# Kernel optimization log

Hardware: AMD Instinct MI355X
Metric: run time of the kernel (lower is better)

Reference implementation:

```python
import jax, jax.numpy as jnp
import numpy as np

N = 50000   # nodes
E = 800000  # edges (before self loops)
F = 128     # in_dim
H = 4       # heads
C = 32      # hidden_dim per head
HC = H * C  # 128 == F
L = 3       # n_layers
G = 64      # graphs in batch
OUT = 64    # out_dim
NEG_SLOPE = 0.2


def setup_inputs() -> dict:
    key = jax.random.key(0)
    ks = jax.random.split(key, 12)
    s = 0.1
    x = jax.random.normal(ks[0], (N, F), jnp.float32)
    src = jax.random.randint(ks[1], (E,), 0, N, dtype=jnp.int32)
    dst = jax.random.randint(ks[2], (E,), 0, N, dtype=jnp.int32)
    # even split into G graphs so no graph is empty (segment_max safe)
    batch = (jnp.arange(N, dtype=jnp.int32) * G // N).astype(jnp.int32)
    Ws = jax.random.normal(ks[3], (L, HC, HC), jnp.float32) * s       # layer0 in=F=HC
    att_src = jax.random.normal(ks[4], (L, H, C), jnp.float32) * s
    att_dst = jax.random.normal(ks[5], (L, H, C), jnp.float32) * s
    conv_b = jnp.zeros((L, HC), jnp.float32)
    gate_W = jax.random.normal(ks[6], (L + 1, HC, 1), jnp.float32) * s
    gate_b = jnp.zeros((L + 1,), jnp.float32)
    lin_W = jax.random.normal(ks[7], (L + 1, HC, OUT), jnp.float32) * s
    lin_b = jnp.zeros((L + 1, OUT), jnp.float32)
    h_weights = jnp.ones((L + 1,), jnp.float32) / (L + 1)
    h0 = jax.random.normal(ks[8], (1,), jnp.float32)
    beta = jax.random.normal(ks[9], (OUT,), jnp.float32) * s
    pool_w = jnp.ones((3,), jnp.float32) / 3.0
    return dict(x=x, src=src, dst=dst, batch=batch, Ws=Ws, att_src=att_src,
                att_dst=att_dst, conv_b=conv_b, gate_W=gate_W, gate_b=gate_b,
                lin_W=lin_W, lin_b=lin_b, h_weights=h_weights, h0=h0,
                beta=beta, pool_w=pool_w)


def _seg_softmax(e, idx, n):
    # numerically stable softmax within segments
    m = jax.ops.segment_max(e, idx, num_segments=n)
    m = jnp.where(jnp.isfinite(m), m, 0.0)
    ex = jnp.exp(e - m[idx])
    s = jax.ops.segment_sum(ex, idx, num_segments=n)
    return ex / (s[idx] + 1e-16)


def _gat_layer(x, src, dst, W, a_src, a_dst, b):
    h = (x @ W).reshape(N, H, C)               # [N,H,C]
    al_s = jnp.sum(h * a_src, axis=-1)         # [N,H]
    al_d = jnp.sum(h * a_dst, axis=-1)         # [N,H]
    e = jax.nn.leaky_relu(al_s[src] + al_d[dst], NEG_SLOPE)  # [E+N,H]
    alpha = _seg_softmax(e, dst, N)            # softmax over incoming edges
    msg = h[src] * alpha[..., None]            # [E+N,H,C]
    out = jax.ops.segment_sum(msg, dst, num_segments=N)
    return out.reshape(N, HC) + b


def _pool_block(x, gw, gb, pool_w, batch, counts):
    gate = jax.nn.sigmoid(x @ gw + gb)[:, 0]          # [N]
    a = _seg_softmax(gate, batch, G)                  # per-graph attention
    p_att = jax.ops.segment_sum(a[:, None] * x, batch, num_segments=G)
    p_mean = jax.ops.segment_sum(x, batch, num_segments=G) / counts[:, None]
    p_max = jax.ops.segment_max(x, batch, num_segments=G)
    return pool_w[0] * p_att + pool_w[1] * p_mean + pool_w[2] * p_max


def reference(x, src, dst, batch, Ws, att_src, att_dst, conv_b, gate_W,
              gate_b, lin_W, lin_b, h_weights, h0, beta, pool_w):
    loops = jnp.arange(N, dtype=src.dtype)
    src_sl = jnp.concatenate([src, loops])
    dst_sl = jnp.concatenate([dst, loops])
    counts = jax.ops.segment_sum(jnp.ones((N,), x.dtype), batch, num_segments=G)
    out = jnp.zeros((G, OUT), x.dtype)
    for i in range(L):
        p = _pool_block(x, gate_W[i], gate_b[i], pool_w, batch, counts)
        out = out + h_weights[i] * (p @ lin_W[i] + lin_b[i])
        x = _gat_layer(x, src_sl, dst_sl, Ws[i], att_src[i], att_dst[i], conv_b[i])
        if i != L - 1:
            x = jax.nn.relu(x)
    p = _pool_block(x, gate_W[L], gate_b[L], pool_w, batch, counts)
    out = out + h_weights[L] * (p @ lin_W[L] + lin_b[L])
    risk_score = out @ beta + h0[0]   # [G]
    return risk_score
```

## Files before the change

### kernel.cpp

```cpp
#include <hip/hip_runtime.h>
#include <hip/hip_fp16.h>
#include <math.h>

#define N_NODES 50000
#define N_EDGES 800000
#define HC 128
#define NH 4
#define NG 64
#define NOUT 64
#define NLAYERS 3
#define POOL_CHUNKS 16
#define CAST_BLOCKS (N_NODES * HC / 4 / 256)
#define PREPW_BLOCKS (NLAYERS * HC * HC / 256)
#define NBKT ((N_NODES + 127) / 128)
#define PB_BLOCKS ((N_EDGES + 4095) / 4096)
#define GEMM_BLOCKS ((N_NODES + 15) / 16)
#define POOL2_BLOCKS (NG * POOL_CHUNKS / 2)
#define XT_STRIDE 136
#define LOG2E 1.44269504f

typedef _Float16 v4h __attribute__((ext_vector_type(4)));
typedef float v4f __attribute__((ext_vector_type(4)));

__device__ __forceinline__ void graph_range(int g, int* start, int* end) {
    *start = (int)(((long long)g * N_NODES + NG - 1) / NG);
    *end   = (int)(((long long)(g + 1) * N_NODES + NG - 1) / NG);
}

__device__ __forceinline__ float atomicMaxFloat(float* addr, float val) {
    if (val >= 0.f)
        return __int_as_float(atomicMax((int*)addr, __float_as_int(val)));
    else
        return __uint_as_float(atomicMin((unsigned int*)addr, __float_as_uint(val)));
}


__device__ __forceinline__ void gemm_body(
        int b, const __half* __restrict__ x, const _Float16* __restrict__ Wt,
        const float* __restrict__ a_src, const float* __restrict__ a_dst,
        __half* __restrict__ hh, float* __restrict__ al_s, float* __restrict__ al_d) {
    __shared__ __align__(16) _Float16 xt[16][XT_STRIDE];
    int t = threadIdx.x;
    int w = t >> 6;
    int l = t & 63;
    int n0 = b * 16;
    {
        uint4 v = ((const uint4*)(x + (size_t)n0 * HC))[t];
        *(uint4*)&xt[t >> 4][(t & 15) * 8] = v;
    }
    __syncthreads();
    int m = l & 15;
    int kg = (l >> 4) * 4;
    v4h a[8];
#pragma unroll
    for (int ks = 0; ks < 8; ks++)
        a[ks] = *(const v4h*)&xt[m][kg + ks * 16];
    __syncthreads();
    const _Float16* bp0 = Wt + (uint)(w * 32 + m) * HC + kg;
    const _Float16* bp1 = bp0 + 16 * HC;
    v4f acc0 = {0.f, 0.f, 0.f, 0.f}, acc1 = {0.f, 0.f, 0.f, 0.f};
#pragma unroll
    for (int ks = 0; ks < 8; ks++) {
        v4h b0 = *(const v4h*)(bp0 + ks * 16);
        v4h b1 = *(const v4h*)(bp1 + ks * 16);
        acc0 = __builtin_amdgcn_mfma_f32_16x16x16f16(a[ks], b0, acc0, 0, 0, 0);
        acc1 = __builtin_amdgcn_mfma_f32_16x16x16f16(a[ks], b1, acc1, 0, 0, 0);
    }
    int d0 = w * 32 + m;
    float as0 = a_src[d0] * LOG2E,      ad0 = a_dst[d0] * LOG2E;
    float as1 = a_src[d0 + 16] * LOG2E, ad1 = a_dst[d0 + 16] * LOG2E;
    int rloc = (l >> 4) * 4;
#pragma unroll
    for (int r = 0; r < 4; r++) {
        int n = n0 + rloc + r;
        xt[rloc + r][d0]      = (_Float16)acc0[r];
        xt[rloc + r][d0 + 16] = (_Float16)acc1[r];
        float vs = acc0[r] * as0 + acc1[r] * as1;
        float vd = acc0[r] * ad0 + acc1[r] * ad1;
#pragma unroll
        for (int mk = 8; mk >= 1; mk >>= 1) {
            vs += __shfl_xor(vs, mk);
            vd += __shfl_xor(vd, mk);
        }
        if ((l & 15) == 0) {
            al_s[(uint)(n * NH + w)] = vs;
            al_d[(uint)(n * NH + w)] = vd;
        }
    }
    __syncthreads();
    uint4 v = *(const uint4*)&xt[t >> 4][(t & 15) * 8];
    ((uint4*)(hh + (size_t)n0 * HC))[t] = v;
}

__device__ __forceinline__ void pool_body(
        int b, const __half* __restrict__ x, const float* __restrict__ gate,
        float* __restrict__ p_att, float* __restrict__ p_sum,
        float* __restrict__ p_max, float* __restrict__ wsum) {
    int c = b * 2 + (threadIdx.x >> 7);
    int g = c >> 4;
    int chunk = c & 15;
    int d = threadIdx.x & 127;
    int start, end; graph_range(g, &start, &end);
    int cnt = end - start;
    int cstart = start + (cnt * chunk) / POOL_CHUNKS;
    int cend   = start + (cnt * (chunk + 1)) / POOL_CHUNKS;
    float aat = 0.f, asu = 0.f, amx = -INFINITY, ws = 0.f;
    int n = cstart;
    for (; n + 4 <= cend; n += 4) {
        float w0 = gate[n],     w1 = gate[n + 1];
        float w2 = gate[n + 2], w3 = gate[n + 3];
        float x0 = __half2float(x[(uint)((n + 0) * HC + d)]);
        float x1 = __half2float(x[(uint)((n + 1) * HC + d)]);
        float x2 = __half2float(x[(uint)((n + 2) * HC + d)]);
        float x3 = __half2float(x[(uint)((n + 3) * HC + d)]);
        aat = fmaf(w0, x0, aat); aat = fmaf(w1, x1, aat);
        aat = fmaf(w2, x2, aat); aat = fmaf(w3, x3, aat);
        asu += (x0 + x1) + (x2 + x3);
        amx = fmaxf(amx, fmaxf(fmaxf(x0, x1), fmaxf(x2, x3)));
        ws += (w0 + w1) + (w2 + w3);
    }
    for (; n < cend; n++) {
        float w = gate[n];
        float xv = __half2float(x[(uint)(n * HC + d)]);
        aat = fmaf(w, xv, aat);
        asu += xv;
        amx = fmaxf(amx, xv);
        ws += w;
    }
    atomicAdd(&p_att[g * HC + d], aat);
    atomicAdd(&p_sum[g * HC + d], asu);
    atomicMaxFloat(&p_max[g * HC + d], amx);
    if (d == 0) atomicAdd(&wsum[g], ws);
}

__device__ __forceinline__ void scat2_body(
        int bkt, const int2* __restrict__ part, const int* __restrict__ bktbase,
        int* __restrict__ rowptr, int* __restrict__ csr_src) {
    __shared__ int degs[128];
    __shared__ int curs[128];
    __shared__ int w0tot;
    int t = threadIdx.x;
    int nstart = bkt << 7;
    int nend = nstart + 128; if (nend > N_NODES) nend = N_NODES;
    int nloc = nend - nstart;
    int estart = bktbase[bkt], eend = bktbase[bkt + 1];
    if (t < 128) degs[t] = 0;
    __syncthreads();
    for (int e = estart + t; e < eend; e += 256)
        atomicAdd(&degs[part[e].y - nstart], 1);
    __syncthreads();
    int v = 0, inc = 0;
    if (t < 128) {
        v = degs[t];
        inc = v;
#pragma unroll
        for (int off = 1; off < 64; off <<= 1) {
            int u = __shfl_up(inc, off);
            if ((t & 63) >= off) inc += u;
        }
    }
    if (t == 63) w0tot = inc;
    __syncthreads();
    if (t < 128) {
        int excl = inc - v + ((t >= 64) ? w0tot : 0);
        int rp = estart + excl;
        curs[t] = rp;
        if (t < nloc) rowptr[nstart + t] = rp;
    }
    __syncthreads();
    for (int e = estart + t; e < eend; e += 256) {
        int2 p = part[e];
        int pos = atomicAdd(&curs[p.y - nstart], 1);
        csr_src[pos] = p.x;
    }
}


__global__ __launch_bounds__(256) void k_prep(
        const float* __restrict__ x, __half* __restrict__ xh,
        const float* __restrict__ Ws, _Float16* __restrict__ Wt,
        const int* __restrict__ dst, int* __restrict__ bh,
        const float* __restrict__ gw, const float* __restrict__ gbp,
        float* __restrict__ gate) {
    int b = blockIdx.x;
    int t = threadIdx.x;
    if (b < CAST_BLOCKS) {
        uint i = b * 256 + t;
        float4 v = ((const float4*)x)[i];
        __half2 a = __floats2half2_rn(v.x, v.y);
        __half2 c = __floats2half2_rn(v.z, v.w);
        ((__half2*)xh)[2 * i] = a;
        ((__half2*)xh)[2 * i + 1] = c;
        float4 gwv = ((const float4*)gw)[t & 31];
        float dot = v.x * gwv.x + v.y * gwv.y + v.z * gwv.z + v.w * gwv.w;
#pragma unroll
        for (int m = 16; m >= 1; m >>= 1) dot += __shfl_xor(dot, m);
        if ((t & 31) == 0) {
            int n = b * 8 + (t >> 5);
            float sg = 1.f / (1.f + __expf(-(dot + gbp[0])));
            gate[n] = __expf(sg);
        }
    } else if (b < CAST_BLOCKS + PREPW_BLOCKS) {
        int e = (b - CAST_BLOCKS) * 256 + t;
        int layer = e >> 14; int r = e & 16383; int k = r >> 7; int d = r & 127;
        Wt[layer * 16384 + d * 128 + k] = (_Float16)Ws[layer * 16384 + k * 128 + d];
    } else {
        int pb = b - CAST_BLOCKS - PREPW_BLOCKS;
        __shared__ int cnt[NBKT];
        for (int i = t; i < NBKT; i += 256) cnt[i] = 0;
        __syncthreads();
        int base = pb * 4096;
#pragma unroll
        for (int k = 0; k < 16; k++) {
            int e = base + t + 256 * k;
            if (e < N_EDGES) atomicAdd(&cnt[dst[e] >> 7], 1);
        }
        __syncthreads();
        for (int i = t; i < NBKT; i += 256) bh[i * PB_BLOCKS + pb] = cnt[i];
    }
}

__global__ __launch_bounds__(256) void k_scan_bh(int* __restrict__ bh,
                                                 int* __restrict__ bkttot) {
    __shared__ int tmp[256];
    int bkt = blockIdx.x, t = threadIdx.x;
    int v = (t < PB_BLOCKS) ? bh[bkt * PB_BLOCKS + t] : 0;
    tmp[t] = v;
    __syncthreads();
    for (int off = 1; off < 256; off <<= 1) {
        int u = (t >= off) ? tmp[t - off] : 0;
        __syncthreads();
        tmp[t] += u;
        __syncthreads();
    }
    if (t < PB_BLOCKS) bh[bkt * PB_BLOCKS + t] = tmp[t] - v;
    if (t == 255) bkttot[bkt] = tmp[255];
}

__global__ __launch_bounds__(512) void k_bktbase(const int* __restrict__ bkttot,
                                                 int* __restrict__ bktbase,
                                                 int* __restrict__ rowptr) {
    __shared__ int tmp[512];
    int t = threadIdx.x;
    int v = (t < NBKT) ? bkttot[t] : 0;
    tmp[t] = v;
    __syncthreads();
    for (int off = 1; off < 512; off <<= 1) {
        int u = (t >= off) ? tmp[t - off] : 0;
        __syncthreads();
        tmp[t] += u;
        __syncthreads();
    }
    if (t < NBKT) bktbase[t] = tmp[t] - v;
    if (t == NBKT - 1) {
        bktbase[NBKT] = tmp[t];
        rowptr[N_NODES] = tmp[t];
    }
}

__global__ __launch_bounds__(256) void k_part(
        const int* __restrict__ src, const int* __restrict__ dst,
        const int* __restrict__ bktbase, const int* __restrict__ bh,
        int2* __restrict__ part) {
    __shared__ int curs[NBKT];
    int blk = blockIdx.x, t = threadIdx.x;
    for (int i = t; i < NBKT; i += 256)
        curs[i] = bktbase[i] + bh[i * PB_BLOCKS + blk];
    __syncthreads();
    int base = blk * 4096;
#pragma unroll
    for (int k = 0; k < 16; k++) {
        int e = base + t + 256 * k;
        if (e < N_EDGES) {
            int d = dst[e];
            int pos = atomicAdd(&curs[d >> 7], 1);
            part[pos] = make_int2(src[e], d);
        }
    }
}


__global__ __launch_bounds__(256) void k_fused_a2(
        const int2* __restrict__ part, const int* __restrict__ bktbase,
        int* __restrict__ rowptr, int* __restrict__ csr_src,
        const __half* __restrict__ x0h, const _Float16* __restrict__ Wt,
        const float* __restrict__ a_src, const float* __restrict__ a_dst,
        __half* __restrict__ hh, float* __restrict__ al_s, float* __restrict__ al_d,
        const float* __restrict__ gate,
        float* __restrict__ p_att, float* __restrict__ p_sum,
        float* __restrict__ p_max, float* __restrict__ wsum) {
    int b = blockIdx.x;
    if (b < NBKT) {
        scat2_body(b, part, bktbase, rowptr, csr_src);
    } else if (b < NBKT + GEMM_BLOCKS) {
        gemm_body(b - NBKT, x0h, Wt, a_src, a_dst, hh, al_s, al_d);
    } else {
        pool_body(b - NBKT - GEMM_BLOCKS, x0h, gate, p_att, p_sum, p_max, wsum);
    }
}

__global__ __launch_bounds__(256) void k_fused_b(
        const __half* __restrict__ x, const _Float16* __restrict__ Wt,
        const float* __restrict__ a_src, const float* __restrict__ a_dst,
        __half* __restrict__ hh, float* __restrict__ al_s, float* __restrict__ al_d,
        const float* __restrict__ gate,
        float* __restrict__ p_att, float* __restrict__ p_sum,
        float* __restrict__ p_max, float* __restrict__ wsum) {
    int b = blockIdx.x;
    if (b < GEMM_BLOCKS) {
        gemm_body(b, x, Wt, a_src, a_dst, hh, al_s, al_d);
    } else {
        pool_body(b - GEMM_BLOCKS, x, gate, p_att, p_sum, p_max, wsum);
    }
}

__global__ __launch_bounds__(256) void k_pool(
        const __half* __restrict__ x, const float* __restrict__ gate,
        float* __restrict__ p_att, float* __restrict__ p_sum,
        float* __restrict__ p_max, float* __restrict__ wsum) {
    pool_body(blockIdx.x, x, gate, p_att, p_sum, p_max, wsum);
}


__global__ __launch_bounds__(256) void k_agg(
        const __half* __restrict__ hh, const float* __restrict__ al_s,
        const float* __restrict__ al_d, const int* __restrict__ rowptr,
        const int* __restrict__ csr_src, const float* __restrict__ conv_b,
        __half* __restrict__ xout, int do_relu,
        const float* __restrict__ gw, const float* __restrict__ gbp,
        float* __restrict__ gate) {
    int n = (blockIdx.x * blockDim.x + threadIdx.x) >> 6;
    if (n >= N_NODES) return;
    int l = threadIdx.x & 63;
    int head = l >> 4;
    int le = l & 15;
    float ad = al_d[(uint)(n * NH + head)];
    const __half2* hh2 = (const __half2*)hh;
    float e0 = al_s[(uint)(n * NH + head)] + ad;
    e0 = fmaxf(e0, 0.2f * e0);
    float s_uni = exp2f(e0);
    float2 vself = __half22float2(hh2[(uint)(n * 64 + l)]);
    float ax = s_uni * vself.x, ay = s_uni * vself.y;
    int jb = rowptr[n], je = rowptr[n + 1];
    int j = jb;
    float s_part = 0.f;
    for (; j + 16 <= je; j += 16) {
        int my_s = csr_src[j + le];
        float aa = al_s[(uint)(my_s * NH + head)];
        float e = aa + ad;
        e = fmaxf(e, 0.2f * e);
        float ex = exp2f(e);
        s_part += ex;
        __half2 vv[16];
#pragma unroll
        for (int u = 0; u < 16; u++) {
            int ssu = __builtin_amdgcn_readlane(my_s, u);
            vv[u] = hh2[(uint)(ssu * 64 + l)];
        }
        int grp = l & 48;
#pragma unroll
        for (int u = 0; u < 16; u++) {
            float exu = __shfl(ex, grp + u);
            float2 vf = __half22float2(vv[u]);
            ax = fmaf(exu, vf.x, ax);
            ay = fmaf(exu, vf.y, ay);
        }
    }
    for (; j + 4 <= je; j += 4) {
        int ss[4];
#pragma unroll
        for (int u = 0; u < 4; u++) ss[u] = csr_src[j + u];
        float aa[4];
#pragma unroll
        for (int u = 0; u < 4; u++) aa[u] = al_s[(uint)(ss[u] * NH + head)];
        __half2 vv[4];
#pragma unroll
        for (int u = 0; u < 4; u++) vv[u] = hh2[(uint)(ss[u] * 64 + l)];
#pragma unroll
        for (int u = 0; u < 4; u++) {
            float e = aa[u] + ad; e = fmaxf(e, 0.2f * e);
            float ex = exp2f(e); s_uni += ex;
            float2 vf = __half22float2(vv[u]);
            ax = fmaf(ex, vf.x, ax); ay = fmaf(ex, vf.y, ay);
        }
    }
    for (; j < je; j++) {
        int s0 = csr_src[j];
        float a0 = al_s[(uint)(s0 * NH + head)];
        __half2 v0 = hh2[(uint)(s0 * 64 + l)];
        float e = a0 + ad; e = fmaxf(e, 0.2f * e);
        float ex = exp2f(e); s_uni += ex;
        float2 vf = __half22float2(v0);
        ax = fmaf(ex, vf.x, ax); ay = fmaf(ex, vf.y, ay);
    }
    s_part += __shfl_xor(s_part, 1);
    s_part += __shfl_xor(s_part, 2);
    s_part += __shfl_xor(s_part, 4);
    s_part += __shfl_xor(s_part, 8);
    float s = s_part + s_uni;
    float inv = 1.f / (s + 1e-16f);
    float2 cb = ((const float2*)conv_b)[l];
    float r0 = fmaf(ax, inv, cb.x);
    float r1 = fmaf(ay, inv, cb.y);
    if (do_relu) { r0 = fmaxf(r0, 0.f); r1 = fmaxf(r1, 0.f); }
    ((__half2*)xout)[(uint)(n * 64 + l)] = __floats2half2_rn(r0, r1);
    float2 gwv = ((const float2*)gw)[l];
    float gv = r0 * gwv.x + r1 * gwv.y;
#pragma unroll
    for (int m = 32; m >= 1; m >>= 1) gv += __shfl_xor(gv, m);
    if (l == 0) {
        float sg = 1.f / (1.f + __expf(-(gv + gbp[0])));
        gate[n] = __expf(sg);
    }
}


__global__ __launch_bounds__(128) void k_finish(
        const float* __restrict__ p_att, const float* __restrict__ p_sum,
        const float* __restrict__ p_max, const float* __restrict__ wsum,
        const float* __restrict__ pool_w, const float* __restrict__ lin_W,
        const float* __restrict__ lin_b, const float* __restrict__ hw,
        const float* __restrict__ beta, const float* __restrict__ h0,
        float* __restrict__ out) {
    int g = blockIdx.x, t = threadIdx.x;
    __shared__ float p[NLAYERS + 1][HC];
    int start, end; graph_range(g, &start, &end);
    float cinv = 1.f / (float)(end - start);
    float pw0 = pool_w[0], pw1 = pool_w[1], pw2 = pool_w[2];
#pragma unroll
    for (int j = 0; j <= NLAYERS; j++) {
        float winv = 1.f / (wsum[j * NG + g] + 1e-16f);
        p[j][t] = pw0 * p_att[(j * NG + g) * HC + t] * winv
                + pw1 * p_sum[(j * NG + g) * HC + t] * cinv
                + pw2 * p_max[(j * NG + g) * HC + t];
    }
    __syncthreads();
    if (t < NOUT) {
        float acc = 0.f;
#pragma unroll
        for (int j = 0; j <= NLAYERS; j++) {
            float a = lin_b[j * NOUT + t];
            const float* Wj = lin_W + (size_t)j * HC * NOUT;
            for (int k = 0; k < HC; k++) a = fmaf(p[j][k], Wj[k * NOUT + t], a);
            acc = fmaf(hw[j], a, acc);
        }
        float v = acc * beta[t];
#pragma unroll
        for (int m = 32; m >= 1; m >>= 1) v += __shfl_xor(v, m);
        if (t == 0) out[g] = v + h0[0];
    }
}


extern "C" void kernel_launch(void* const* d_in, const int* in_sizes, int n_in,
                              void* d_out, int out_size, void* d_ws, size_t ws_size,
                              hipStream_t stream) {
    const float* x0       = (const float*)d_in[0];
    const int*   src      = (const int*)d_in[1];
    const int*   dst      = (const int*)d_in[2];
    const float* Ws       = (const float*)d_in[4];
    const float* att_src  = (const float*)d_in[5];
    const float* att_dst  = (const float*)d_in[6];
    const float* conv_b   = (const float*)d_in[7];
    const float* gate_W   = (const float*)d_in[8];
    const float* gate_b   = (const float*)d_in[9];
    const float* lin_W    = (const float*)d_in[10];
    const float* lin_b    = (const float*)d_in[11];
    const float* h_w      = (const float*)d_in[12];
    const float* h0       = (const float*)d_in[13];
    const float* beta     = (const float*)d_in[14];
    const float* pool_w   = (const float*)d_in[15];

    char* base = (char*)d_ws;
    size_t off = 0;
    auto carve = [&](size_t bytes) -> char* {
        char* p = base + off;
        off = (off + bytes + 255) & ~(size_t)255;
        return p;
    };
    __half*    x0h     = (__half*)carve((size_t)N_NODES * HC * 2);
    __half*    xA      = (__half*)carve((size_t)N_NODES * HC * 2);
    __half*    xB      = (__half*)carve((size_t)N_NODES * HC * 2);
    __half*    hh      = (__half*)carve((size_t)N_NODES * HC * 2);
    _Float16*  Wt      = (_Float16*)carve((size_t)NLAYERS * HC * HC * 2);
    float*     al_s    = (float*)carve((size_t)N_NODES * NH * 4);
    float*     al_d    = (float*)carve((size_t)N_NODES * NH * 4);
    float*     gate    = (float*)carve((size_t)N_NODES * 4);
    int*       rowptr  = (int*)carve((size_t)(N_NODES + 1) * 4);
    int*       csrsrc  = (int*)carve((size_t)N_EDGES * 4);
    int*       bh      = (int*)carve((size_t)NBKT * PB_BLOCKS * 4);
    int*       bkttot  = (int*)carve((size_t)NBKT * 4);
    int*       bktbase = (int*)carve((size_t)(NBKT + 1) * 4);
    int2*      part    = (int2*)carve((size_t)N_EDGES * 8);
    size_t zfloats = (size_t)(NLAYERS + 1) * NG * HC * 2 + (NLAYERS + 1) * NG;
    float*     zreg    = (float*)carve(zfloats * 4);
    float*     p_att   = zreg;
    float*     p_sum   = zreg + (size_t)(NLAYERS + 1) * NG * HC;
    float*     wsum    = p_sum + (size_t)(NLAYERS + 1) * NG * HC;
    float*     p_max   = (float*)carve((size_t)(NLAYERS + 1) * NG * HC * 4);

    hipMemsetAsync(zreg, 0, zfloats * 4, stream);
    hipMemsetAsync(p_max, 0xFF, (size_t)(NLAYERS + 1) * NG * HC * 4, stream);

    k_prep<<<CAST_BLOCKS + PREPW_BLOCKS + PB_BLOCKS, 256, 0, stream>>>(
        x0, x0h, Ws, Wt, dst, bh, gate_W, gate_b, gate);

    k_scan_bh<<<NBKT, 256, 0, stream>>>(bh, bkttot);
    k_bktbase<<<1, 512, 0, stream>>>(bkttot, bktbase, rowptr);
    k_part<<<PB_BLOCKS, 256, 0, stream>>>(src, dst, bktbase, bh, part);

    k_fused_a2<<<NBKT + GEMM_BLOCKS + POOL2_BLOCKS, 256, 0, stream>>>(
        part, bktbase, rowptr, csrsrc,
        x0h, Wt, att_src, att_dst, hh, al_s, al_d,
        gate, p_att, p_sum, p_max, wsum);

    __half* xbufs[3] = { xA, xB, xA };
    for (int i = 0; i < NLAYERS; i++) {
        __half* xnext = xbufs[i];
        int j = i + 1;
        k_agg<<<(N_NODES + 3) / 4, 256, 0, stream>>>(hh, al_s, al_d, rowptr, csrsrc,
                                                     conv_b + i * HC, xnext,
                                                     (i != NLAYERS - 1) ? 1 : 0,
                                                     gate_W + j * HC, gate_b + j,
                                                     gate);
        if (i + 1 < NLAYERS) {
            k_fused_b<<<GEMM_BLOCKS + POOL2_BLOCKS, 256, 0, stream>>>(
                xnext, Wt + (size_t)(i + 1) * HC * HC,
                att_src + (i + 1) * HC, att_dst + (i + 1) * HC,
                hh, al_s, al_d,
                gate,
                p_att + (size_t)j * NG * HC,
                p_sum + (size_t)j * NG * HC,
                p_max + (size_t)j * NG * HC,
                wsum + j * NG);
        } else {
            k_pool<<<POOL2_BLOCKS, 256, 0, stream>>>(
                xnext, gate,
                p_att + (size_t)j * NG * HC,
                p_sum + (size_t)j * NG * HC,
                p_max + (size_t)j * NG * HC,
                wsum + j * NG);
        }
    }

    k_finish<<<NG, 128, 0, stream>>>(p_att, p_sum, p_max, wsum, pool_w,
                                     lin_W, lin_b, h_w, beta, h0, (float*)d_out);
}
```

Measured before the change: 294.1 us.

## Fold buffer memsets into prep kernel and unify agg edge loop with masked tail

Replaces the two hipMemsetAsync calls that zero the pooling accumulators and fill p_max with extra blocks in the k_prep launch, removing two separate operations from the stream. In k_agg the 4-wide and scalar remainder loops are dropped; all edges go through the 16-wide loop, with lanes past the end masked to zero weight. The cross-lane broadcast now uses ds_bpermute directly, and gather addresses are computed with 64-bit offsets. Masked tails waste some gather work on short rows, since every tail still issues 16 loads.

```diff
diff --git a/kernel.cpp b/kernel.cpp
--- a/kernel.cpp
+++ b/kernel.cpp
@@ -17,6 +17,9 @@
 #define GEMM_BLOCKS ((N_NODES + 15) / 16)
 #define POOL2_BLOCKS (NG * POOL_CHUNKS / 2)
 #define XT_STRIDE 136
+#define ZREG_FLOATS ((NLAYERS + 1) * NG * HC * 2 + (NLAYERS + 1) * NG)
+#define ZREG_BLOCKS ((ZREG_FLOATS / 4 + 255) / 256)
+#define PMAX_BLOCKS ((NLAYERS + 1) * NG * HC / 4 / 256)
 #define LOG2E 1.44269504f
 
 typedef _Float16 v4h __attribute__((ext_vector_type(4)));
@@ -181,7 +184,8 @@
         const float* __restrict__ Ws, _Float16* __restrict__ Wt,
         const int* __restrict__ dst, int* __restrict__ bh,
         const float* __restrict__ gw, const float* __restrict__ gbp,
-        float* __restrict__ gate) {
+        float* __restrict__ gate,
+        float* __restrict__ zreg, uint* __restrict__ pmaxw) {
     int b = blockIdx.x;
     int t = threadIdx.x;
     if (b < CAST_BLOCKS) {
@@ -204,7 +208,7 @@
         int e = (b - CAST_BLOCKS) * 256 + t;
         int layer = e >> 14; int r = e & 16383; int k = r >> 7; int d = r & 127;
         Wt[layer * 16384 + d * 128 + k] = (_Float16)Ws[layer * 16384 + k * 128 + d];
-    } else {
+    } else if (b < CAST_BLOCKS + PREPW_BLOCKS + PB_BLOCKS) {
         int pb = b - CAST_BLOCKS - PREPW_BLOCKS;
         __shared__ int cnt[NBKT];
         for (int i = t; i < NBKT; i += 256) cnt[i] = 0;
@@ -217,6 +221,17 @@
         }
         __syncthreads();
         for (int i = t; i < NBKT; i += 256) bh[i * PB_BLOCKS + pb] = cnt[i];
+    } else {
+        int zb = b - CAST_BLOCKS - PREPW_BLOCKS - PB_BLOCKS;
+        if (zb < ZREG_BLOCKS) {
+            int i = zb * 256 + t;
+            if (i < ZREG_FLOATS / 4)
+                ((float4*)zreg)[i] = make_float4(0.f, 0.f, 0.f, 0.f);
+        } else {
+            int i = (zb - ZREG_BLOCKS) * 256 + t;
+            uint4 f; f.x = f.y = f.z = f.w = 0xFFFFFFFFu;
+            ((uint4*)pmaxw)[i] = f;
+        }
     }
 }
 
@@ -334,6 +349,7 @@
     int l = threadIdx.x & 63;
     int head = l >> 4;
     int le = l & 15;
+    int grp4 = (l & 48) << 2;
     float ad = al_d[(uint)(n * NH + head)];
     const __half2* hh2 = (const __half2*)hh;
     float e0 = al_s[(uint)(n * NH + head)] + ad;
@@ -342,56 +358,32 @@
     float2 vself = __half22float2(hh2[(uint)(n * 64 + l)]);
     float ax = s_uni * vself.x, ay = s_uni * vself.y;
     int jb = rowptr[n], je = rowptr[n + 1];
-    int j = jb;
     float s_part = 0.f;
-    for (; j + 16 <= je; j += 16) {
-        int my_s = csr_src[j + le];
+    for (int j = jb; j < je; j += 16) {
+        int rem = je - j;
+        bool act = le < rem;
+        int my_s = csr_src[j + (act ? le : 0)];
         float aa = al_s[(uint)(my_s * NH + head)];
         float e = aa + ad;
         e = fmaxf(e, 0.2f * e);
-        float ex = exp2f(e);
+        float ex = act ? exp2f(e) : 0.f;
         s_part += ex;
+        int exb = __float_as_int(ex);
         __half2 vv[16];
 #pragma unroll
         for (int u = 0; u < 16; u++) {
             int ssu = __builtin_amdgcn_readlane(my_s, u);
-            vv[u] = hh2[(uint)(ssu * 64 + l)];
-        }
-        int grp = l & 48;
+            const __half2* rp = hh2 + ((size_t)(uint)ssu << 6);
+            vv[u] = rp[l];
+        }
 #pragma unroll
         for (int u = 0; u < 16; u++) {
-            float exu = __shfl(ex, grp + u);
+            float exu = __int_as_float(
+                __builtin_amdgcn_ds_bpermute(grp4 + 4 * u, exb));
             float2 vf = __half22float2(vv[u]);
             ax = fmaf(exu, vf.x, ax);
             ay = fmaf(exu, vf.y, ay);
         }
-    }
-    for (; j + 4 <= je; j += 4) {
-        int ss[4];
-#pragma unroll
-        for (int u = 0; u < 4; u++) ss[u] = csr_src[j + u];
-        float aa[4];
-#pragma unroll
-        for (int u = 0; u < 4; u++) aa[u] = al_s[(uint)(ss[u] * NH + head)];
-        __half2 vv[4];
-#pragma unroll
-        for (int u = 0; u < 4; u++) vv[u] = hh2[(uint)(ss[u] * 64 + l)];
-#pragma unroll
-        for (int u = 0; u < 4; u++) {
-            float e = aa[u] + ad; e = fmaxf(e, 0.2f * e);
-            float ex = exp2f(e); s_uni += ex;
-            float2 vf = __half22float2(vv[u]);
-            ax = fmaf(ex, vf.x, ax); ay = fmaf(ex, vf.y, ay);
-        }
-    }
-    for (; j < je; j++) {
-        int s0 = csr_src[j];
-        float a0 = al_s[(uint)(s0 * NH + head)];
-        __half2 v0 = hh2[(uint)(s0 * 64 + l)];
-        float e = a0 + ad; e = fmaxf(e, 0.2f * e);
-        float ex = exp2f(e); s_uni += ex;
-        float2 vf = __half22float2(v0);
-        ax = fmaf(ex, vf.x, ax); ay = fmaf(ex, vf.y, ay);
     }
     s_part += __shfl_xor(s_part, 1);
     s_part += __shfl_xor(s_part, 2);
@@ -492,18 +484,15 @@
     int*       bkttot  = (int*)carve((size_t)NBKT * 4);
     int*       bktbase = (int*)carve((size_t)(NBKT + 1) * 4);
     int2*      part    = (int2*)carve((size_t)N_EDGES * 8);
-    size_t zfloats = (size_t)(NLAYERS + 1) * NG * HC * 2 + (NLAYERS + 1) * NG;
-    float*     zreg    = (float*)carve(zfloats * 4);
+    float*     zreg    = (float*)carve((size_t)ZREG_FLOATS * 4);
     float*     p_att   = zreg;
     float*     p_sum   = zreg + (size_t)(NLAYERS + 1) * NG * HC;
     float*     wsum    = p_sum + (size_t)(NLAYERS + 1) * NG * HC;
     float*     p_max   = (float*)carve((size_t)(NLAYERS + 1) * NG * HC * 4);
 
-    hipMemsetAsync(zreg, 0, zfloats * 4, stream);
-    hipMemsetAsync(p_max, 0xFF, (size_t)(NLAYERS + 1) * NG * HC * 4, stream);
-
-    k_prep<<<CAST_BLOCKS + PREPW_BLOCKS + PB_BLOCKS, 256, 0, stream>>>(
-        x0, x0h, Ws, Wt, dst, bh, gate_W, gate_b, gate);
+    k_prep<<<CAST_BLOCKS + PREPW_BLOCKS + PB_BLOCKS + ZREG_BLOCKS + PMAX_BLOCKS,
+             256, 0, stream>>>(
+        x0, x0h, Ws, Wt, dst, bh, gate_W, gate_b, gate, zreg, (uint*)p_max);
 
     k_scan_bh<<<NBKT, 256, 0, stream>>>(bh, bkttot);
     k_bktbase<<<1, 512, 0, stream>>>(bkttot, bktbase, rowptr);
```

New measurement: 270.9 us. 1.09x faster.
